# Optimization experiments

Measured on AMD Instinct MI355X. Metric: run time of the kernel, lower is better.

## Reference

```python
import jax, jax.numpy as jnp
import numpy as np

MARGIN = 0.3
IN_FEATURES = 128
NUM_CLASSES = 100
BATCH = 4096


def setup_inputs() -> dict:
    key = jax.random.key(0)
    k1, k2, k3, k4 = jax.random.split(key, 4)
    embeddings = jax.random.normal(k1, (BATCH, IN_FEATURES), dtype=jnp.float32)
    labels = jax.random.randint(k2, (BATCH,), 0, NUM_CLASSES, dtype=jnp.int64)
    # nn.Linear params (kaiming-uniform-ish scale)
    bound = 1.0 / np.sqrt(IN_FEATURES)
    fc_w = jax.random.uniform(k3, (NUM_CLASSES, IN_FEATURES), jnp.float32, -bound, bound)
    fc_b = jax.random.uniform(k4, (NUM_CLASSES,), jnp.float32, -bound, bound)
    return {"embeddings": embeddings, "labels": labels, "fc_w": fc_w, "fc_b": fc_b}


def _triplet_hard(emb, labels, margin):
    # pairwise squared euclidean distances: ||a||^2 + ||b||^2 - 2 a.b
    sq = jnp.sum(emb * emb, axis=1)  # [B]
    d2 = sq[:, None] + sq[None, :] - 2.0 * (emb @ emb.T)
    dist = jnp.sqrt(jnp.clip(d2, 1e-12))  # [B, B]
    same = labels[:, None] == labels[None, :]  # [B, B] (diag True, as in torch)
    neg_inf = jnp.float32(-jnp.inf)
    pos_inf = jnp.float32(jnp.inf)
    ap = jnp.max(jnp.where(same, dist, neg_inf), axis=1)  # hardest positive
    an = jnp.min(jnp.where(same, pos_inf, dist), axis=1)  # hardest negative
    # MarginRankingLoss(target=1): mean(relu(-(an - ap) + margin))
    return jnp.mean(jax.nn.relu(ap - an + margin))


def _cross_entropy(logits, labels):
    logp = jax.nn.log_softmax(logits, axis=-1)
    return -jnp.mean(jnp.take_along_axis(logp, labels[:, None], axis=1)[:, 0])


def reference(embeddings, labels, fc_w, fc_b):
    logits = embeddings @ fc_w.T + fc_b  # [B, C]
    triplet = _triplet_hard(embeddings, labels, MARGIN)
    ce = _cross_entropy(logits, labels)
    return triplet + ce
```

## Files before the change

### kernel.cpp

```cpp
#include <hip/hip_runtime.h>
#include <math.h>

#define BATCH 4096
#define DIM 128
#define NCLS 100
#define MARGIN 0.3f
#define NTILE 272
#define GRID_ALL 272
#define POISON 0xAAAAAAAAu

typedef __attribute__((ext_vector_type(8))) short short8;
typedef __attribute__((ext_vector_type(4))) float f32x4;

__device__ __forceinline__ unsigned short f2bf(float f) {
    unsigned int u = __float_as_uint(f);
    unsigned int r = (u + 0x7FFFu + ((u >> 16) & 1u)) >> 16;
    return (unsigned short)r;
}
__device__ __forceinline__ float bf2f(unsigned short b) {
    return __uint_as_float(((unsigned int)b) << 16);
}

#define ENC_MAX_ID 0x80000000u
#define ENC_MIN_ID 0x403FFFFFu
__device__ __forceinline__ unsigned int enc_max(float v) {
    return (__float_as_uint(v) >> 1) | 0x80000000u;
}
__device__ __forceinline__ float dec_max(unsigned int k) {
    return __uint_as_float((k & 0x7FFFFFFFu) << 1);
}
__device__ __forceinline__ unsigned int enc_min(float v) {
    return 0x7FFFFFFFu - (__float_as_uint(v) >> 1);
}
__device__ __forceinline__ float dec_min(unsigned int k) {
    return __uint_as_float((0x7FFFFFFFu - k) << 1);
}

__device__ __forceinline__ void st_u32(unsigned int* p, unsigned int v) {
    __hip_atomic_store(p, v, __ATOMIC_RELAXED, __HIP_MEMORY_SCOPE_AGENT);
}
__device__ __forceinline__ void st_f32(float* p, float v) {
    __hip_atomic_store(p, v, __ATOMIC_RELAXED, __HIP_MEMORY_SCOPE_AGENT);
}


__global__ __launch_bounds__(256, 2) void fused_kernel(
        const float* __restrict__ emb, const int* __restrict__ labels,
        const float* __restrict__ fcw, const float* __restrict__ fcb,
        float* __restrict__ out,
        unsigned short* __restrict__ ebf, unsigned short* __restrict__ wbf,
        float* __restrict__ sq,
        unsigned int* __restrict__ maxk, unsigned int* __restrict__ mink,
        float* __restrict__ ce_sum, int* __restrict__ ticket,
        unsigned int* __restrict__ fanz, unsigned int* __restrict__ prep_ticket) {
    __shared__ float lg[16][128];
    __shared__ unsigned int colk[512];
    __shared__ unsigned short bstage[2][2048];
    __shared__ int lastFlag;
    int bid = blockIdx.x, tid = threadIdx.x;
    int wave = tid >> 6, lane = tid & 63;
    int lm = lane & 15, lq = lane >> 4;

    if (bid < 256) {
        unsigned int* dstg = reinterpret_cast<unsigned int*>(ebf) + bid * 1024;
        #pragma unroll
        for (int r = 0; r < 4; ++r) {
            int rowl = wave * 4 + r;
            int row = bid * 16 + rowl;
            const float2* src = reinterpret_cast<const float2*>(emb + row * DIM);
            float2 xy = src[lane];
            unsigned short b0 = f2bf(xy.x), b1 = f2bf(xy.y);
            float y0 = bf2f(b0), y1 = bf2f(b1);
            st_u32(&dstg[(lane >> 2) * 64 + rowl * 4 + (lane & 3)],
                   ((unsigned int)b1 << 16) | (unsigned int)b0);
            float acc = y0 * y0 + y1 * y1;
            #pragma unroll
            for (int off = 1; off < 64; off <<= 1) acc += __shfl_xor(acc, off, 64);
            if (lane == 0) st_f32(&sq[row], acc);
        }
    } else {
        int idx = (bid - 256) * 256 + tid;
        unsigned int* wbf32 = reinterpret_cast<unsigned int*>(wbf);
        for (int t = idx; t < 7168; t += 4096) {
            int k = t * 2;
            int cls = k >> 7, d = k & 127;
            unsigned int packed = 0;
            if (k < NCLS * DIM)
                packed = ((unsigned int)f2bf(fcw[k + 1]) << 16) | (unsigned int)f2bf(fcw[k]);
            int dst = (cls >> 4) * 2048 + (d >> 3) * 128 + (cls & 15) * 8 + (d & 7);
            st_u32(&wbf32[dst >> 1], packed);
        }
        for (int w = idx; w < 8194; w += 4096)
            st_u32(&fanz[w], 0u);
    }
    asm volatile("s_waitcnt vmcnt(0)" ::: "memory");
    __syncthreads();
    if (tid == 0) {
        unsigned int exp = POISON;
        __hip_atomic_compare_exchange_strong(prep_ticket, &exp, 0u,
                                             __ATOMIC_RELAXED, __ATOMIC_RELAXED,
                                             __HIP_MEMORY_SCOPE_AGENT);
        __hip_atomic_fetch_add(prep_ticket, 1u,
                               __ATOMIC_RELAXED, __HIP_MEMORY_SCOPE_AGENT);
        while (__hip_atomic_load(prep_ticket, __ATOMIC_RELAXED,
                                 __HIP_MEMORY_SCOPE_AGENT) < GRID_ALL)
            __builtin_amdgcn_s_sleep(8);
    }
    __syncthreads();

    {
        int c = 0, rem = bid;
        while (rem >= 2 * c + 2) { rem -= 2 * c + 2; ++c; }
        int rowgrp = rem, chunk = c;

        int rbase = rowgrp * 128 + wave * 32;
        const unsigned short* apt = ebf + (rbase >> 4) * 2048 + lane * 8;
        short8 a0 = *reinterpret_cast<const short8*>(apt);
        short8 a1 = *reinterpret_cast<const short8*>(apt + 512);
        short8 a2 = *reinterpret_cast<const short8*>(apt + 1024);
        short8 a3 = *reinterpret_cast<const short8*>(apt + 1536);
        short8 a4 = *reinterpret_cast<const short8*>(apt + 2048);
        short8 a5 = *reinterpret_cast<const short8*>(apt + 2560);
        short8 a6 = *reinterpret_cast<const short8*>(apt + 3072);
        short8 a7 = *reinterpret_cast<const short8*>(apt + 3584);

        int labr[8];
        float sqr[8];
        #pragma unroll
        for (int g = 0; g < 2; ++g)
            #pragma unroll
            for (int r = 0; r < 4; ++r) {
                labr[g * 4 + r] = labels[rbase + g * 16 + lq * 4 + r];
                sqr[g * 4 + r]  = sq[rbase + g * 16 + lq * 4 + r];
            }

        colk[tid] = 0; colk[256 + tid] = 0;

        float rmax[8], rmin[8];
        #pragma unroll
        for (int r = 0; r < 8; ++r) { rmax[r] = -INFINITY; rmin[r] = INFINITY; }

        int cbase = chunk * 256;
        const unsigned short* btile = ebf + (cbase >> 4) * 2048 + wave * 512 + lane * 8;
        uint4 breg = *reinterpret_cast<const uint4*>(btile);

        for (int ct = 0; ct < 16; ++ct) {
            *reinterpret_cast<uint4*>(&bstage[ct & 1][wave * 512 + lane * 8]) = breg;
            if (ct < 15)
                breg = *reinterpret_cast<const uint4*>(btile + (ct + 1) * 2048);
            __syncthreads();

            const unsigned short* bb = &bstage[ct & 1][lane * 8];
            short8 b0 = *reinterpret_cast<const short8*>(bb);
            short8 b1 = *reinterpret_cast<const short8*>(bb + 512);
            short8 b2 = *reinterpret_cast<const short8*>(bb + 1024);
            short8 b3 = *reinterpret_cast<const short8*>(bb + 1536);
            f32x4 c0 = {0.f, 0.f, 0.f, 0.f};
            f32x4 c1 = {0.f, 0.f, 0.f, 0.f};
            c0 = __builtin_amdgcn_mfma_f32_16x16x32_bf16(a0, b0, c0, 0, 0, 0);
            c1 = __builtin_amdgcn_mfma_f32_16x16x32_bf16(a4, b0, c1, 0, 0, 0);
            c0 = __builtin_amdgcn_mfma_f32_16x16x32_bf16(a1, b1, c0, 0, 0, 0);
            c1 = __builtin_amdgcn_mfma_f32_16x16x32_bf16(a5, b1, c1, 0, 0, 0);
            c0 = __builtin_amdgcn_mfma_f32_16x16x32_bf16(a2, b2, c0, 0, 0, 0);
            c1 = __builtin_amdgcn_mfma_f32_16x16x32_bf16(a6, b2, c1, 0, 0, 0);
            c0 = __builtin_amdgcn_mfma_f32_16x16x32_bf16(a3, b3, c0, 0, 0, 0);
            c1 = __builtin_amdgcn_mfma_f32_16x16x32_bf16(a7, b3, c1, 0, 0, 0);

            int col = cbase + ct * 16 + lm;
            float sqc = sq[col];
            int lc = labels[col];
            float cmax = -INFINITY, cmin = INFINITY;
            #pragma unroll
            for (int r = 0; r < 4; ++r) {
                float v0 = fmaxf(fmaf(c0[r], -2.0f, sqc) + sqr[r], 0.f);
                bool s0 = (lc == labr[r]);
                rmax[r] = s0 ? fmaxf(rmax[r], v0) : rmax[r];
                rmin[r] = s0 ? rmin[r] : fminf(rmin[r], v0);
                cmax    = s0 ? fmaxf(cmax, v0) : cmax;
                cmin    = s0 ? cmin : fminf(cmin, v0);
                float v1 = fmaxf(fmaf(c1[r], -2.0f, sqc) + sqr[4 + r], 0.f);
                bool s1 = (lc == labr[4 + r]);
                rmax[4 + r] = s1 ? fmaxf(rmax[4 + r], v1) : rmax[4 + r];
                rmin[4 + r] = s1 ? rmin[4 + r] : fminf(rmin[4 + r], v1);
                cmax        = s1 ? fmaxf(cmax, v1) : cmax;
                cmin        = s1 ? cmin : fminf(cmin, v1);
            }
            cmax = fmaxf(cmax, __shfl_xor(cmax, 16, 64));
            cmax = fmaxf(cmax, __shfl_xor(cmax, 32, 64));
            cmin = fminf(cmin, __shfl_xor(cmin, 16, 64));
            cmin = fminf(cmin, __shfl_xor(cmin, 32, 64));
            if (lq == 0) {
                atomicMax(&colk[ct * 16 + lm], enc_max(fmaxf(cmax, 0.f)));
                atomicMax(&colk[256 + ct * 16 + lm], enc_min(fmaxf(cmin, 0.f)));
            }
        }
        #pragma unroll
        for (int off = 1; off < 16; off <<= 1) {
            #pragma unroll
            for (int r = 0; r < 8; ++r) {
                rmax[r] = fmaxf(rmax[r], __shfl_xor(rmax[r], off, 64));
                rmin[r] = fminf(rmin[r], __shfl_xor(rmin[r], off, 64));
            }
        }
        if (lm == 0) {
            #pragma unroll
            for (int g = 0; g < 2; ++g)
                #pragma unroll
                for (int r = 0; r < 4; ++r) {
                    int row = rbase + g * 16 + lq * 4 + r;
                    unsigned int kx = enc_max(fmaxf(rmax[g * 4 + r], 0.f));
                    unsigned int kn = enc_min(fmaxf(rmin[g * 4 + r], 0.f));
                    if (kx != ENC_MAX_ID)
                        __hip_atomic_fetch_max(&maxk[row], kx,
                                               __ATOMIC_RELAXED, __HIP_MEMORY_SCOPE_AGENT);
                    if (kn != ENC_MIN_ID)
                        __hip_atomic_fetch_max(&mink[row], kn,
                                               __ATOMIC_RELAXED, __HIP_MEMORY_SCOPE_AGENT);
                }
        }
        __syncthreads();
        {
            unsigned int kx = colk[tid], kn = colk[256 + tid];
            int col = cbase + tid;
            if (kx > ENC_MAX_ID)
                __hip_atomic_fetch_max(&maxk[col], kx,
                                       __ATOMIC_RELAXED, __HIP_MEMORY_SCOPE_AGENT);
            if (kn != 0 && kn != ENC_MIN_ID)
                __hip_atomic_fetch_max(&mink[col], kn,
                                       __ATOMIC_RELAXED, __HIP_MEMORY_SCOPE_AGENT);
        }
    }

    if (bid < 256) {
        int R0 = bid * 16;
        __syncthreads();
        lg[tid >> 4][112 + (tid & 15)] = -INFINITY;

        const unsigned short* apt = ebf + (R0 >> 4) * 2048 + lane * 8;
        short8 a0 = *reinterpret_cast<const short8*>(apt);
        short8 a1 = *reinterpret_cast<const short8*>(apt + 512);
        short8 a2 = *reinterpret_cast<const short8*>(apt + 1024);
        short8 a3 = *reinterpret_cast<const short8*>(apt + 1536);

        for (int t = wave * 2; t < 7 && t < wave * 2 + 2; ++t) {
            int cls = t * 16 + lm;
            const unsigned short* bp = wbf + t * 2048 + lane * 8;
            short8 b0 = *reinterpret_cast<const short8*>(bp);
            short8 b1 = *reinterpret_cast<const short8*>(bp + 512);
            short8 b2 = *reinterpret_cast<const short8*>(bp + 1024);
            short8 b3 = *reinterpret_cast<const short8*>(bp + 1536);
            f32x4 c = {0.f, 0.f, 0.f, 0.f};
            c = __builtin_amdgcn_mfma_f32_16x16x32_bf16(a0, b0, c, 0, 0, 0);
            c = __builtin_amdgcn_mfma_f32_16x16x32_bf16(a1, b1, c, 0, 0, 0);
            c = __builtin_amdgcn_mfma_f32_16x16x32_bf16(a2, b2, c, 0, 0, 0);
            c = __builtin_amdgcn_mfma_f32_16x16x32_bf16(a3, b3, c, 0, 0, 0);
            float bias = (cls < NCLS) ? fcb[cls] : -INFINITY;
            #pragma unroll
            for (int r = 0; r < 4; ++r)
                lg[lq * 4 + r][t * 16 + lm] = c[r] + bias;
        }
        __syncthreads();
        float cacc = 0.f;
        #pragma unroll
        for (int i = 0; i < 4; ++i) {
            int r = wave * 4 + i;
            float x0 = lg[r][lane], x1 = lg[r][lane + 64];
            float m = fmaxf(x0, x1);
            #pragma unroll
            for (int off = 1; off < 64; off <<= 1) m = fmaxf(m, __shfl_xor(m, off, 64));
            float s = expf(x0 - m) + expf(x1 - m);
            #pragma unroll
            for (int off = 1; off < 64; off <<= 1) s += __shfl_xor(s, off, 64);
            if (lane == 0) {
                int lab = labels[R0 + r];
                cacc += (m + logf(s)) - lg[r][lab];
            }
        }
        __syncthreads();
        if (lane == 0) lg[0][wave] = cacc;
        __syncthreads();
        if (tid == 0) {
            float bsum = lg[0][0] + lg[0][1] + lg[0][2] + lg[0][3];
            __hip_atomic_fetch_add(ce_sum, bsum,
                                   __ATOMIC_RELAXED, __HIP_MEMORY_SCOPE_AGENT);
        }
    }

    __syncthreads();
    asm volatile("s_waitcnt vmcnt(0)" ::: "memory");
    if (tid == 0) {
        int old = __hip_atomic_fetch_add(ticket, 1,
                                         __ATOMIC_RELAXED, __HIP_MEMORY_SCOPE_AGENT);
        lastFlag = (old == GRID_ALL - 1);
    }
    __syncthreads();
    if (lastFlag) {
        float acc = 0.f;
        #pragma unroll
        for (int rr = 0; rr < 16; ++rr) {
            int row = rr * 256 + tid;
            unsigned int kx = __hip_atomic_load(&maxk[row], __ATOMIC_RELAXED,
                                                __HIP_MEMORY_SCOPE_AGENT);
            unsigned int kn = __hip_atomic_load(&mink[row], __ATOMIC_RELAXED,
                                                __HIP_MEMORY_SCOPE_AGENT);
            float ap = sqrtf(fmaxf(dec_max(kx), 1e-12f));
            float an = sqrtf(fmaxf(dec_min(kn), 1e-12f));
            acc += fmaxf(ap - an + MARGIN, 0.f);
        }
        float* red = reinterpret_cast<float*>(lg);
        red[tid] = acc;
        __syncthreads();
        for (int s = 128; s > 0; s >>= 1) {
            if (tid < s) red[tid] += red[tid + s];
            __syncthreads();
        }
        if (tid == 0) {
            float ces = __hip_atomic_load(ce_sum, __ATOMIC_RELAXED,
                                          __HIP_MEMORY_SCOPE_AGENT);
            out[0] = (red[0] + ces) * (1.0f / BATCH);
        }
    }
}

extern "C" void kernel_launch(void* const* d_in, const int* in_sizes, int n_in,
                              void* d_out, int out_size, void* d_ws, size_t ws_size,
                              hipStream_t stream) {
    const float* emb    = (const float*)d_in[0];
    const int*   labels = (const int*)  d_in[1];
    const float* fcw    = (const float*)d_in[2];
    const float* fcb    = (const float*)d_in[3];
    float* out = (float*)d_out;

    char* ws = (char*)d_ws;
    unsigned short* ebf = (unsigned short*)(ws);
    unsigned short* wbf = (unsigned short*)(ws + 1048576);
    float* sq           = (float*)(ws + 1081344);
    char* fan           = ws + 1097728;
    int*   ticket       = (int*)(fan);
    float* ce_sum       = (float*)(fan + 4);
    unsigned int* maxk  = (unsigned int*)(fan + 8);
    unsigned int* mink  = (unsigned int*)(fan + 8 + 16384);
    unsigned int* prep_ticket = (unsigned int*)(fan + 8 + 32768);

    fused_kernel<<<GRID_ALL, 256, 0, stream>>>(
        emb, labels, fcw, fcb, out, ebf, wbf, sq,
        maxk, mink, ce_sum, ticket, (unsigned int*)fan, prep_ticket);
}
```

Before: 99.94 us.

## Remove grid-wide prep barrier by converting fp32 to bf16 on the fly per block

Drops the separate prep phase that wrote bf16 embeddings, bf16 FC weights and squared norms to global workspace, along with the grid-wide barrier that waited on it. Each block now loads fp32 embeddings directly, converts them to bf16 in registers, and computes row and column squared norms locally through shuffles and LDS. The FC weight tile is converted per block into LDS. Block 0 zeroes the accumulators and sets a magic flag that other blocks wait on only before their global atomics. The cost is redundant conversion work across blocks, more fp32 global reads, and a larger LDS footprint.

```diff
diff --git a/kernel.cpp b/kernel.cpp
--- a/kernel.cpp
+++ b/kernel.cpp
@@ -7,7 +7,7 @@
 #define MARGIN 0.3f
 #define NTILE 272
 #define GRID_ALL 272
-#define POISON 0xAAAAAAAAu
+#define MAGIC 0x13572468u
 
 typedef __attribute__((ext_vector_type(8))) short short8;
 typedef __attribute__((ext_vector_type(4))) float f32x4;
@@ -39,225 +39,226 @@
 __device__ __forceinline__ void st_u32(unsigned int* p, unsigned int v) {
     __hip_atomic_store(p, v, __ATOMIC_RELAXED, __HIP_MEMORY_SCOPE_AGENT);
 }
-__device__ __forceinline__ void st_f32(float* p, float v) {
-    __hip_atomic_store(p, v, __ATOMIC_RELAXED, __HIP_MEMORY_SCOPE_AGENT);
-}
-
+
+__device__ __forceinline__ short8 cvt8(const float* __restrict__ p, float& ss) {
+    float4 x = *reinterpret_cast<const float4*>(p);
+    float4 y = *reinterpret_cast<const float4*>(p + 4);
+    unsigned short h0 = f2bf(x.x), h1 = f2bf(x.y), h2 = f2bf(x.z), h3 = f2bf(x.w);
+    unsigned short h4 = f2bf(y.x), h5 = f2bf(y.y), h6 = f2bf(y.z), h7 = f2bf(y.w);
+    float r0 = bf2f(h0), r1 = bf2f(h1), r2 = bf2f(h2), r3 = bf2f(h3);
+    float r4 = bf2f(h4), r5 = bf2f(h5), r6 = bf2f(h6), r7 = bf2f(h7);
+    ss += r0 * r0 + r1 * r1 + r2 * r2 + r3 * r3 + r4 * r4 + r5 * r5 + r6 * r6 + r7 * r7;
+    short8 o;
+    o[0] = (short)h0; o[1] = (short)h1; o[2] = (short)h2; o[3] = (short)h3;
+    o[4] = (short)h4; o[5] = (short)h5; o[6] = (short)h6; o[7] = (short)h7;
+    return o;
+}
 
 __global__ __launch_bounds__(256, 2) void fused_kernel(
         const float* __restrict__ emb, const int* __restrict__ labels,
         const float* __restrict__ fcw, const float* __restrict__ fcb,
         float* __restrict__ out,
-        unsigned short* __restrict__ ebf, unsigned short* __restrict__ wbf,
-        float* __restrict__ sq,
         unsigned int* __restrict__ maxk, unsigned int* __restrict__ mink,
         float* __restrict__ ce_sum, int* __restrict__ ticket,
-        unsigned int* __restrict__ fanz, unsigned int* __restrict__ prep_ticket) {
+        unsigned int* __restrict__ flag, unsigned int* __restrict__ fanz) {
     __shared__ float lg[16][128];
     __shared__ unsigned int colk[512];
     __shared__ unsigned short bstage[2][2048];
+    __shared__ unsigned short wlds[7 * 2048];
+    __shared__ float sqpart[2][4][16];
+    __shared__ float sqrowL[4][2][16];
     __shared__ int lastFlag;
     int bid = blockIdx.x, tid = threadIdx.x;
     int wave = tid >> 6, lane = tid & 63;
     int lm = lane & 15, lq = lane >> 4;
 
+    if (bid == 0) {
+        for (int w = tid; w < 8194; w += 256) st_u32(&fanz[w], 0u);
+        asm volatile("s_waitcnt vmcnt(0)" ::: "memory");
+        __syncthreads();
+        if (tid == 0) st_u32(flag, MAGIC);
+    }
+
+    int c = 0, rem = bid;
+    while (rem >= 2 * c + 2) { rem -= 2 * c + 2; ++c; }
+    int rowgrp = rem, chunk = c;
+    int rbase = rowgrp * 128 + wave * 32;
+    int cbase = chunk * 256;
+
+    short8 afr[2][4];
+    #pragma unroll
+    for (int g = 0; g < 2; ++g) {
+        int row = rbase + g * 16 + lm;
+        const float* base = emb + row * DIM + lq * 8;
+        float ss = 0.f;
+        #pragma unroll
+        for (int j = 0; j < 4; ++j) afr[g][j] = cvt8(base + j * 32, ss);
+        ss += __shfl_xor(ss, 16, 64);
+        ss += __shfl_xor(ss, 32, 64);
+        if (lq == 0) sqrowL[wave][g][lm] = ss;
+    }
+
+    int labr[8];
+    #pragma unroll
+    for (int g = 0; g < 2; ++g)
+        #pragma unroll
+        for (int r = 0; r < 4; ++r)
+            labr[g * 4 + r] = labels[rbase + g * 16 + lq * 4 + r];
+
+    colk[tid] = 0; colk[256 + tid] = 0;
+    __syncthreads();
+
+    float sqr[8];
+    #pragma unroll
+    for (int g = 0; g < 2; ++g)
+        #pragma unroll
+        for (int r = 0; r < 4; ++r)
+            sqr[g * 4 + r] = sqrowL[wave][g][lq * 4 + r];
+
+    float rmax[8], rmin[8];
+    #pragma unroll
+    for (int r = 0; r < 8; ++r) { rmax[r] = -INFINITY; rmin[r] = INFINITY; }
+
+    int s = wave * 512 + lane * 8;
+    int bc = s >> 7;
+    int browl = (s >> 3) & 15;
+    const float* bsrc0 = emb + (cbase + browl) * DIM + bc * 8;
+
+    for (int ct = 0; ct < 16; ++ct) {
+        float ssb = 0.f;
+        short8 bq = cvt8(bsrc0 + ct * 16 * DIM, ssb);
+        *reinterpret_cast<short8*>(&bstage[ct & 1][s]) = bq;
+        ssb += __shfl_xor(ssb, 16, 64);
+        ssb += __shfl_xor(ssb, 32, 64);
+        if (lq == 0) sqpart[ct & 1][wave][lm] = ssb;
+        __syncthreads();
+
+        const unsigned short* bb = &bstage[ct & 1][lane * 8];
+        short8 b0 = *reinterpret_cast<const short8*>(bb);
+        short8 b1 = *reinterpret_cast<const short8*>(bb + 512);
+        short8 b2 = *reinterpret_cast<const short8*>(bb + 1024);
+        short8 b3 = *reinterpret_cast<const short8*>(bb + 1536);
+        f32x4 c0 = {0.f, 0.f, 0.f, 0.f};
+        f32x4 c1 = {0.f, 0.f, 0.f, 0.f};
+        c0 = __builtin_amdgcn_mfma_f32_16x16x32_bf16(afr[0][0], b0, c0, 0, 0, 0);
+        c1 = __builtin_amdgcn_mfma_f32_16x16x32_bf16(afr[1][0], b0, c1, 0, 0, 0);
+        c0 = __builtin_amdgcn_mfma_f32_16x16x32_bf16(afr[0][1], b1, c0, 0, 0, 0);
+        c1 = __builtin_amdgcn_mfma_f32_16x16x32_bf16(afr[1][1], b1, c1, 0, 0, 0);
+        c0 = __builtin_amdgcn_mfma_f32_16x16x32_bf16(afr[0][2], b2, c0, 0, 0, 0);
+        c1 = __builtin_amdgcn_mfma_f32_16x16x32_bf16(afr[1][2], b2, c1, 0, 0, 0);
+        c0 = __builtin_amdgcn_mfma_f32_16x16x32_bf16(afr[0][3], b3, c0, 0, 0, 0);
+        c1 = __builtin_amdgcn_mfma_f32_16x16x32_bf16(afr[1][3], b3, c1, 0, 0, 0);
+
+        int col = cbase + ct * 16 + lm;
+        float sqc = sqpart[ct & 1][0][lm] + sqpart[ct & 1][1][lm]
+                  + sqpart[ct & 1][2][lm] + sqpart[ct & 1][3][lm];
+        int lc = labels[col];
+        float cmax = -INFINITY, cmin = INFINITY;
+        #pragma unroll
+        for (int r = 0; r < 4; ++r) {
+            float v0 = fmaxf(fmaf(c0[r], -2.0f, sqc) + sqr[r], 0.f);
+            bool s0 = (lc == labr[r]);
+            rmax[r] = s0 ? fmaxf(rmax[r], v0) : rmax[r];
+            rmin[r] = s0 ? rmin[r] : fminf(rmin[r], v0);
+            cmax    = s0 ? fmaxf(cmax, v0) : cmax;
+            cmin    = s0 ? cmin : fminf(cmin, v0);
+            float v1 = fmaxf(fmaf(c1[r], -2.0f, sqc) + sqr[4 + r], 0.f);
+            bool s1 = (lc == labr[4 + r]);
+            rmax[4 + r] = s1 ? fmaxf(rmax[4 + r], v1) : rmax[4 + r];
+            rmin[4 + r] = s1 ? rmin[4 + r] : fminf(rmin[4 + r], v1);
+            cmax        = s1 ? fmaxf(cmax, v1) : cmax;
+            cmin        = s1 ? cmin : fminf(cmin, v1);
+        }
+        cmax = fmaxf(cmax, __shfl_xor(cmax, 16, 64));
+        cmax = fmaxf(cmax, __shfl_xor(cmax, 32, 64));
+        cmin = fminf(cmin, __shfl_xor(cmin, 16, 64));
+        cmin = fminf(cmin, __shfl_xor(cmin, 32, 64));
+        if (lq == 0) {
+            atomicMax(&colk[ct * 16 + lm], enc_max(fmaxf(cmax, 0.f)));
+            atomicMax(&colk[256 + ct * 16 + lm], enc_min(fmaxf(cmin, 0.f)));
+        }
+    }
+    #pragma unroll
+    for (int off = 1; off < 16; off <<= 1) {
+        #pragma unroll
+        for (int r = 0; r < 8; ++r) {
+            rmax[r] = fmaxf(rmax[r], __shfl_xor(rmax[r], off, 64));
+            rmin[r] = fminf(rmin[r], __shfl_xor(rmin[r], off, 64));
+        }
+    }
+
+    if (tid == 0) {
+        while (__hip_atomic_load(flag, __ATOMIC_RELAXED,
+                                 __HIP_MEMORY_SCOPE_AGENT) != MAGIC)
+            __builtin_amdgcn_s_sleep(2);
+    }
+    __syncthreads();
+
+    if (lm == 0) {
+        #pragma unroll
+        for (int g = 0; g < 2; ++g)
+            #pragma unroll
+            for (int r = 0; r < 4; ++r) {
+                int row = rbase + g * 16 + lq * 4 + r;
+                unsigned int kx = enc_max(fmaxf(rmax[g * 4 + r], 0.f));
+                unsigned int kn = enc_min(fmaxf(rmin[g * 4 + r], 0.f));
+                if (kx != ENC_MAX_ID)
+                    __hip_atomic_fetch_max(&maxk[row], kx,
+                                           __ATOMIC_RELAXED, __HIP_MEMORY_SCOPE_AGENT);
+                if (kn != ENC_MIN_ID)
+                    __hip_atomic_fetch_max(&mink[row], kn,
+                                           __ATOMIC_RELAXED, __HIP_MEMORY_SCOPE_AGENT);
+            }
+    }
+    __syncthreads();
+    {
+        unsigned int kx = colk[tid], kn = colk[256 + tid];
+        int col = cbase + tid;
+        if (kx > ENC_MAX_ID)
+            __hip_atomic_fetch_max(&maxk[col], kx,
+                                   __ATOMIC_RELAXED, __HIP_MEMORY_SCOPE_AGENT);
+        if (kn != 0 && kn != ENC_MIN_ID)
+            __hip_atomic_fetch_max(&mink[col], kn,
+                                   __ATOMIC_RELAXED, __HIP_MEMORY_SCOPE_AGENT);
+    }
+
     if (bid < 256) {
-        unsigned int* dstg = reinterpret_cast<unsigned int*>(ebf) + bid * 1024;
-        #pragma unroll
-        for (int r = 0; r < 4; ++r) {
-            int rowl = wave * 4 + r;
-            int row = bid * 16 + rowl;
-            const float2* src = reinterpret_cast<const float2*>(emb + row * DIM);
-            float2 xy = src[lane];
-            unsigned short b0 = f2bf(xy.x), b1 = f2bf(xy.y);
-            float y0 = bf2f(b0), y1 = bf2f(b1);
-            st_u32(&dstg[(lane >> 2) * 64 + rowl * 4 + (lane & 3)],
-                   ((unsigned int)b1 << 16) | (unsigned int)b0);
-            float acc = y0 * y0 + y1 * y1;
-            #pragma unroll
-            for (int off = 1; off < 64; off <<= 1) acc += __shfl_xor(acc, off, 64);
-            if (lane == 0) st_f32(&sq[row], acc);
-        }
-    } else {
-        int idx = (bid - 256) * 256 + tid;
-        unsigned int* wbf32 = reinterpret_cast<unsigned int*>(wbf);
-        for (int t = idx; t < 7168; t += 4096) {
+        int R0 = bid * 16;
+        unsigned int* w32 = reinterpret_cast<unsigned int*>(wlds);
+        for (int t = tid; t < 7168; t += 256) {
             int k = t * 2;
             int cls = k >> 7, d = k & 127;
             unsigned int packed = 0;
             if (k < NCLS * DIM)
                 packed = ((unsigned int)f2bf(fcw[k + 1]) << 16) | (unsigned int)f2bf(fcw[k]);
             int dst = (cls >> 4) * 2048 + (d >> 3) * 128 + (cls & 15) * 8 + (d & 7);
-            st_u32(&wbf32[dst >> 1], packed);
-        }
-        for (int w = idx; w < 8194; w += 4096)
-            st_u32(&fanz[w], 0u);
-    }
-    asm volatile("s_waitcnt vmcnt(0)" ::: "memory");
-    __syncthreads();
-    if (tid == 0) {
-        unsigned int exp = POISON;
-        __hip_atomic_compare_exchange_strong(prep_ticket, &exp, 0u,
-                                             __ATOMIC_RELAXED, __ATOMIC_RELAXED,
-                                             __HIP_MEMORY_SCOPE_AGENT);
-        __hip_atomic_fetch_add(prep_ticket, 1u,
-                               __ATOMIC_RELAXED, __HIP_MEMORY_SCOPE_AGENT);
-        while (__hip_atomic_load(prep_ticket, __ATOMIC_RELAXED,
-                                 __HIP_MEMORY_SCOPE_AGENT) < GRID_ALL)
-            __builtin_amdgcn_s_sleep(8);
-    }
-    __syncthreads();
-
-    {
-        int c = 0, rem = bid;
-        while (rem >= 2 * c + 2) { rem -= 2 * c + 2; ++c; }
-        int rowgrp = rem, chunk = c;
-
-        int rbase = rowgrp * 128 + wave * 32;
-        const unsigned short* apt = ebf + (rbase >> 4) * 2048 + lane * 8;
-        short8 a0 = *reinterpret_cast<const short8*>(apt);
-        short8 a1 = *reinterpret_cast<const short8*>(apt + 512);
-        short8 a2 = *reinterpret_cast<const short8*>(apt + 1024);
-        short8 a3 = *reinterpret_cast<const short8*>(apt + 1536);
-        short8 a4 = *reinterpret_cast<const short8*>(apt + 2048);
-        short8 a5 = *reinterpret_cast<const short8*>(apt + 2560);
-        short8 a6 = *reinterpret_cast<const short8*>(apt + 3072);
-        short8 a7 = *reinterpret_cast<const short8*>(apt + 3584);
-
-        int labr[8];
-        float sqr[8];
-        #pragma unroll
-        for (int g = 0; g < 2; ++g)
-            #pragma unroll
-            for (int r = 0; r < 4; ++r) {
-                labr[g * 4 + r] = labels[rbase + g * 16 + lq * 4 + r];
-                sqr[g * 4 + r]  = sq[rbase + g * 16 + lq * 4 + r];
-            }
-
-        colk[tid] = 0; colk[256 + tid] = 0;
-
-        float rmax[8], rmin[8];
-        #pragma unroll
-        for (int r = 0; r < 8; ++r) { rmax[r] = -INFINITY; rmin[r] = INFINITY; }
-
-        int cbase = chunk * 256;
-        const unsigned short* btile = ebf + (cbase >> 4) * 2048 + wave * 512 + lane * 8;
-        uint4 breg = *reinterpret_cast<const uint4*>(btile);
-
-        for (int ct = 0; ct < 16; ++ct) {
-            *reinterpret_cast<uint4*>(&bstage[ct & 1][wave * 512 + lane * 8]) = breg;
-            if (ct < 15)
-                breg = *reinterpret_cast<const uint4*>(btile + (ct + 1) * 2048);
-            __syncthreads();
-
-            const unsigned short* bb = &bstage[ct & 1][lane * 8];
-            short8 b0 = *reinterpret_cast<const short8*>(bb);
-            short8 b1 = *reinterpret_cast<const short8*>(bb + 512);
-            short8 b2 = *reinterpret_cast<const short8*>(bb + 1024);
-            short8 b3 = *reinterpret_cast<const short8*>(bb + 1536);
-            f32x4 c0 = {0.f, 0.f, 0.f, 0.f};
-            f32x4 c1 = {0.f, 0.f, 0.f, 0.f};
-            c0 = __builtin_amdgcn_mfma_f32_16x16x32_bf16(a0, b0, c0, 0, 0, 0);
-            c1 = __builtin_amdgcn_mfma_f32_16x16x32_bf16(a4, b0, c1, 0, 0, 0);
-            c0 = __builtin_amdgcn_mfma_f32_16x16x32_bf16(a1, b1, c0, 0, 0, 0);
-            c1 = __builtin_amdgcn_mfma_f32_16x16x32_bf16(a5, b1, c1, 0, 0, 0);
-            c0 = __builtin_amdgcn_mfma_f32_16x16x32_bf16(a2, b2, c0, 0, 0, 0);
-            c1 = __builtin_amdgcn_mfma_f32_16x16x32_bf16(a6, b2, c1, 0, 0, 0);
-            c0 = __builtin_amdgcn_mfma_f32_16x16x32_bf16(a3, b3, c0, 0, 0, 0);
-            c1 = __builtin_amdgcn_mfma_f32_16x16x32_bf16(a7, b3, c1, 0, 0, 0);
-
-            int col = cbase + ct * 16 + lm;
-            float sqc = sq[col];
-            int lc = labels[col];
-            float cmax = -INFINITY, cmin = INFINITY;
-            #pragma unroll
-            for (int r = 0; r < 4; ++r) {
-                float v0 = fmaxf(fmaf(c0[r], -2.0f, sqc) + sqr[r], 0.f);
-                bool s0 = (lc == labr[r]);
-                rmax[r] = s0 ? fmaxf(rmax[r], v0) : rmax[r];
-                rmin[r] = s0 ? rmin[r] : fminf(rmin[r], v0);
-                cmax    = s0 ? fmaxf(cmax, v0) : cmax;
-                cmin    = s0 ? cmin : fminf(cmin, v0);
-                float v1 = fmaxf(fmaf(c1[r], -2.0f, sqc) + sqr[4 + r], 0.f);
-                bool s1 = (lc == labr[4 + r]);
-                rmax[4 + r] = s1 ? fmaxf(rmax[4 + r], v1) : rmax[4 + r];
-                rmin[4 + r] = s1 ? rmin[4 + r] : fminf(rmin[4 + r], v1);
-                cmax        = s1 ? fmaxf(cmax, v1) : cmax;
-                cmin        = s1 ? cmin : fminf(cmin, v1);
-            }
-            cmax = fmaxf(cmax, __shfl_xor(cmax, 16, 64));
-            cmax = fmaxf(cmax, __shfl_xor(cmax, 32, 64));
-            cmin = fminf(cmin, __shfl_xor(cmin, 16, 64));
-            cmin = fminf(cmin, __shfl_xor(cmin, 32, 64));
-            if (lq == 0) {
-                atomicMax(&colk[ct * 16 + lm], enc_max(fmaxf(cmax, 0.f)));
-                atomicMax(&colk[256 + ct * 16 + lm], enc_min(fmaxf(cmin, 0.f)));
-            }
-        }
-        #pragma unroll
-        for (int off = 1; off < 16; off <<= 1) {
-            #pragma unroll
-            for (int r = 0; r < 8; ++r) {
-                rmax[r] = fmaxf(rmax[r], __shfl_xor(rmax[r], off, 64));
-                rmin[r] = fminf(rmin[r], __shfl_xor(rmin[r], off, 64));
-            }
-        }
-        if (lm == 0) {
-            #pragma unroll
-            for (int g = 0; g < 2; ++g)
-                #pragma unroll
-                for (int r = 0; r < 4; ++r) {
-                    int row = rbase + g * 16 + lq * 4 + r;
-                    unsigned int kx = enc_max(fmaxf(rmax[g * 4 + r], 0.f));
-                    unsigned int kn = enc_min(fmaxf(rmin[g * 4 + r], 0.f));
-                    if (kx != ENC_MAX_ID)
-                        __hip_atomic_fetch_max(&maxk[row], kx,
-                                               __ATOMIC_RELAXED, __HIP_MEMORY_SCOPE_AGENT);
-                    if (kn != ENC_MIN_ID)
-                        __hip_atomic_fetch_max(&mink[row], kn,
-                                               __ATOMIC_RELAXED, __HIP_MEMORY_SCOPE_AGENT);
-                }
-        }
-        __syncthreads();
-        {
-            unsigned int kx = colk[tid], kn = colk[256 + tid];
-            int col = cbase + tid;
-            if (kx > ENC_MAX_ID)
-                __hip_atomic_fetch_max(&maxk[col], kx,
-                                       __ATOMIC_RELAXED, __HIP_MEMORY_SCOPE_AGENT);
-            if (kn != 0 && kn != ENC_MIN_ID)
-                __hip_atomic_fetch_max(&mink[col], kn,
-                                       __ATOMIC_RELAXED, __HIP_MEMORY_SCOPE_AGENT);
-        }
-    }
-
-    if (bid < 256) {
-        int R0 = bid * 16;
-        __syncthreads();
+            w32[dst >> 1] = packed;
+        }
+        float dummy = 0.f;
+        const float* base = emb + (R0 + lm) * DIM + lq * 8;
+        short8 ca0 = cvt8(base, dummy);
+        short8 ca1 = cvt8(base + 32, dummy);
+        short8 ca2 = cvt8(base + 64, dummy);
+        short8 ca3 = cvt8(base + 96, dummy);
         lg[tid >> 4][112 + (tid & 15)] = -INFINITY;
-
-        const unsigned short* apt = ebf + (R0 >> 4) * 2048 + lane * 8;
-        short8 a0 = *reinterpret_cast<const short8*>(apt);
-        short8 a1 = *reinterpret_cast<const short8*>(apt + 512);
-        short8 a2 = *reinterpret_cast<const short8*>(apt + 1024);
-        short8 a3 = *reinterpret_cast<const short8*>(apt + 1536);
+        __syncthreads();
 
         for (int t = wave * 2; t < 7 && t < wave * 2 + 2; ++t) {
             int cls = t * 16 + lm;
-            const unsigned short* bp = wbf + t * 2048 + lane * 8;
+            const unsigned short* bp = wlds + t * 2048 + lane * 8;
             short8 b0 = *reinterpret_cast<const short8*>(bp);
             short8 b1 = *reinterpret_cast<const short8*>(bp + 512);
             short8 b2 = *reinterpret_cast<const short8*>(bp + 1024);
             short8 b3 = *reinterpret_cast<const short8*>(bp + 1536);
-            f32x4 c = {0.f, 0.f, 0.f, 0.f};
-            c = __builtin_amdgcn_mfma_f32_16x16x32_bf16(a0, b0, c, 0, 0, 0);
-            c = __builtin_amdgcn_mfma_f32_16x16x32_bf16(a1, b1, c, 0, 0, 0);
-            c = __builtin_amdgcn_mfma_f32_16x16x32_bf16(a2, b2, c, 0, 0, 0);
-            c = __builtin_amdgcn_mfma_f32_16x16x32_bf16(a3, b3, c, 0, 0, 0);
+            f32x4 cc = {0.f, 0.f, 0.f, 0.f};
+            cc = __builtin_amdgcn_mfma_f32_16x16x32_bf16(ca0, b0, cc, 0, 0, 0);
+            cc = __builtin_amdgcn_mfma_f32_16x16x32_bf16(ca1, b1, cc, 0, 0, 0);
+            cc = __builtin_amdgcn_mfma_f32_16x16x32_bf16(ca2, b2, cc, 0, 0, 0);
+            cc = __builtin_amdgcn_mfma_f32_16x16x32_bf16(ca3, b3, cc, 0, 0, 0);
             float bias = (cls < NCLS) ? fcb[cls] : -INFINITY;
             #pragma unroll
             for (int r = 0; r < 4; ++r)
-                lg[lq * 4 + r][t * 16 + lm] = c[r] + bias;
+                lg[lq * 4 + r][t * 16 + lm] = cc[r] + bias;
         }
         __syncthreads();
         float cacc = 0.f;
@@ -268,12 +269,12 @@
             float m = fmaxf(x0, x1);
             #pragma unroll
             for (int off = 1; off < 64; off <<= 1) m = fmaxf(m, __shfl_xor(m, off, 64));
-            float s = expf(x0 - m) + expf(x1 - m);
+            float ssum = expf(x0 - m) + expf(x1 - m);
             #pragma unroll
-            for (int off = 1; off < 64; off <<= 1) s += __shfl_xor(s, off, 64);
+            for (int off = 1; off < 64; off <<= 1) ssum += __shfl_xor(ssum, off, 64);
             if (lane == 0) {
                 int lab = labels[R0 + r];
-                cacc += (m + logf(s)) - lg[r][lab];
+                cacc += (m + logf(ssum)) - lg[r][lab];
             }
         }
         __syncthreads();
@@ -310,8 +311,8 @@
         float* red = reinterpret_cast<float*>(lg);
         red[tid] = acc;
         __syncthreads();
-        for (int s = 128; s > 0; s >>= 1) {
-            if (tid < s) red[tid] += red[tid + s];
+        for (int st = 128; st > 0; st >>= 1) {
+            if (tid < st) red[tid] += red[tid + st];
             __syncthreads();
         }
         if (tid == 0) {
@@ -331,18 +332,14 @@
     const float* fcb    = (const float*)d_in[3];
     float* out = (float*)d_out;
 
-    char* ws = (char*)d_ws;
-    unsigned short* ebf = (unsigned short*)(ws);
-    unsigned short* wbf = (unsigned short*)(ws + 1048576);
-    float* sq           = (float*)(ws + 1081344);
-    char* fan           = ws + 1097728;
+    char* fan = (char*)d_ws;
     int*   ticket       = (int*)(fan);
     float* ce_sum       = (float*)(fan + 4);
     unsigned int* maxk  = (unsigned int*)(fan + 8);
     unsigned int* mink  = (unsigned int*)(fan + 8 + 16384);
-    unsigned int* prep_ticket = (unsigned int*)(fan + 8 + 32768);
+    unsigned int* flag  = (unsigned int*)(fan + 8 + 32768);
 
     fused_kernel<<<GRID_ALL, 256, 0, stream>>>(
-        emb, labels, fcw, fcb, out, ebf, wbf, sq,
-        maxk, mink, ce_sum, ticket, (unsigned int*)fan, prep_ticket);
-}
+        emb, labels, fcw, fcb, out, maxk, mink, ce_sum, ticket, flag,
+        (unsigned int*)fan);
+}
```

Result: slower. 102.0 us (+2.1%).
